# Optimization experiments

Hardware: AMD Instinct MI355X
Metric: run time of the kernel (lower is better)

The kernel has to match this reference:

```python
import jax, jax.numpy as jnp
import numpy as np

H = 8        # attention heads
EPS = 1e-5   # LayerNorm eps (torch default)


def _ln(x, g, b):
    m = x.mean(-1, keepdims=True)
    v = ((x - m) ** 2).mean(-1, keepdims=True)
    return (x - m) / jnp.sqrt(v + EPS) * g + b


def _mha(q, k, v):
    # q,k,v: [B, A, S, D] -> attend over S within each (B, A); D = H * dh
    Bq, A, S, Dm = q.shape
    dh = Dm // H
    q = q.reshape(Bq, A, S, H, dh)
    k = k.reshape(Bq, A, S, H, dh)
    v = v.reshape(Bq, A, S, H, dh)
    sc = jnp.einsum('bashe,bathe->bahst', q, k) / jnp.sqrt(jnp.asarray(dh, q.dtype))
    a = jax.nn.softmax(sc, axis=-1)
    o = jnp.einsum('bahst,bathe->bashe', a, v)
    return o.reshape(Bq, A, S, Dm)


def setup_inputs() -> dict:
    Ps, B, C, L, D, DF, PRED = 6, 16, 8, 64, 512, 2048, 96
    key = jax.random.key(0)
    ks = jax.random.split(key, 16)
    g = lambda k, s: jax.random.normal(k, s, jnp.float32) * 0.02
    D2 = (D, D)
    return dict(
        expert_x=jax.random.normal(ks[0], (Ps, B, C, L, D), jnp.float32),
        gates=jax.random.uniform(ks[1], (B, Ps), dtype=jnp.float32),
        cWq=g(ks[2], D2), cbq=jnp.zeros(D), cWk=g(ks[3], D2), cbk=jnp.zeros(D),
        cWv=g(ks[4], D2), cbv=jnp.zeros(D), cWo=g(ks[5], D2), cbo=jnp.zeros(D),
        iWq=g(ks[6], D2), ibq=jnp.zeros(D), iWk=g(ks[7], D2), ibk=jnp.zeros(D),
        iWv=g(ks[8], D2), ibv=jnp.zeros(D), iWo=g(ks[9], D2), ibo=jnp.zeros(D),
        mW1=g(ks[10], (D, DF)), mb1=jnp.zeros(DF),
        mW2=g(ks[11], (DF, D)), mb2=jnp.zeros(D),
        g1=jnp.ones(D), b1=jnp.zeros(D),
        g3=jnp.ones(D), b3=jnp.zeros(D),
        g4=jnp.ones(D), b4=jnp.zeros(D),
        hW=g(ks[12], (D, PRED)), hb=jnp.zeros(PRED),
    )


def reference(expert_x, gates,
              cWq, cbq, cWk, cbk, cWv, cbv, cWo, cbo,
              iWq, ibq, iWk, ibk, iWv, ibv, iWo, ibo,
              mW1, mb1, mW2, mb2,
              g1, b1, g3, b3, g4, b4,
              hW, hb):
    def layer(x):  # x: [B, C, L, D]
        # cross-dimension attention block (attend along L per channel)
        q = x @ cWq + cbq
        k = x @ cWk + cbk
        v = x @ cWv + cbv
        o = _mha(q, k, v) @ cWo + cbo
        x = _ln(x + o, g1, b1)
        # inter-periodicity attention block (rearrange B C L D -> B L C D, attend along C)
        q = (x @ iWq + ibq).swapaxes(1, 2)
        k = (x @ iWk + ibk).swapaxes(1, 2)
        v = (x @ iWv + ibv).swapaxes(1, 2)
        o = _mha(q, k, v).swapaxes(1, 2) @ iWo + ibo
        x = _ln(x + o, g3, b3)
        # inter-periodicity MLP (relu) + residual + norm4
        h = jnp.maximum(x @ mW1 + mb1, 0.0) @ mW2 + mb2
        return _ln(x + h, g4, b4)

    enc = jax.vmap(layer)(expert_x)                      # [Ps, B, C, L, D]
    last = enc[:, :, :, -1, :]                           # [Ps, B, C, D]: xs[i][:, :, -1:, :]
    combined = jnp.einsum('pbcd,bp->bcd', last, gates)   # gated combine over experts
    out = combined @ hW + hb                             # [B, C, pred_len]
    return out.transpose(0, 2, 1)                        # [B, pred_len, C]
```

## Files before the change

### kernel.cpp

```cpp
#include <hip/hip_runtime.h>
#include <hip/hip_bf16.h>

#define NT   49152
#define D_   512
#define DF_  2048
#define PS   6
#define BB   16
#define CC   8
#define LL   64
#define PREDN 96
#define NG   768

typedef unsigned short ushort_t;
using bf16x8 = __attribute__((ext_vector_type(8))) short;
using f32x4  = __attribute__((ext_vector_type(4))) float;

__device__ __forceinline__ float bf2f(unsigned short u) {
  return __uint_as_float((unsigned)u << 16);
}
__device__ __forceinline__ unsigned short f2bf(float f) {
  unsigned u = __float_as_uint(f);
  return (unsigned short)((u + 0x7fffu + ((u >> 16) & 1u)) >> 16);
}
__device__ __forceinline__ void unp2(int x, float& a, float& b) {
  a = __uint_as_float((unsigned)x << 16);
  b = __uint_as_float((unsigned)x & 0xffff0000u);
}
__device__ __forceinline__ void gload16(const void* g, void* l) {
  __builtin_amdgcn_global_load_lds(
      (const __attribute__((address_space(1))) unsigned*)g,
      (__attribute__((address_space(3))) unsigned*)l, 16, 0, 0);
}

template <bool RELU, bool DIAGA>
__global__ __launch_bounds__(512, 2) void gemm_mfma(
    const ushort_t* __restrict__ A,
    const ushort_t* __restrict__ Bt,
    const float* __restrict__ bias,
    ushort_t* __restrict__ C,
    int M, int N, int K) {
  __shared__ __align__(16) char smem[73728];
  short* lds = (short*)smem;
  const int tid = threadIdx.x;
  const int lane = tid & 63;
  const int w = tid >> 6;
  const int wm = w >> 1;
  const int wn = w & 1;
  const int l15 = lane & 15, l4 = lane >> 4;

  const int nbn = N >> 7;
  const int nwg = gridDim.x;
  const int qq = nwg >> 3, rr = nwg & 7;
  const int xcd = blockIdx.x & 7, within = blockIdx.x >> 3;
  const int wg = (xcd < rr ? xcd * (qq + 1) : rr * (qq + 1) + (xcd - rr) * qq) + within;
  const int bn = (wg % nbn) << 7;
  const int bm = (wg / nbn) << 8;

  const int NKT = K >> 5;

  const int ciA0 = w * 64 + lane;
  const int ciA1 = 512 + w * 64 + lane;
  const int ciB  = w * 64 + lane;
  const int rA0 = ciA0 >> 2, rA1 = ciA1 >> 2, rB = ciB >> 2;
  const int jA0 = (ciA0 & 3) ^ ((rA0 >> 1) & 3);
  const int jA1 = (ciA1 & 3) ^ ((rA1 >> 1) & 3);
  const int jB  = (ciB  & 3) ^ ((rB  >> 1) & 3);
  const ushort_t* gA0 = A + (size_t)(bm + rA0) * K + (jA0 << 3);
  const ushort_t* gA1 = A + (size_t)(bm + rA1) * K + (jA1 << 3);
  const ushort_t* gB  = Bt + (size_t)(bn + rB) * K + (jB << 3);

  auto stage = [&](int st, int sb) {
    const int k0 = st << 5;
    if (DIAGA) {
      const int kk0 = k0 + (jA0 << 3);
      const int kk1 = k0 + (jA1 << 3);
      gload16(A + ((size_t)(bm + rA0) * 8 + (kk0 >> 6)) * 512 + kk0,
              smem + sb * 24576 + w * 1024);
      gload16(A + ((size_t)(bm + rA1) * 8 + (kk1 >> 6)) * 512 + kk1,
              smem + sb * 24576 + 8192 + w * 1024);
    } else {
      gload16(gA0 + k0, smem + sb * 24576 + w * 1024);
      gload16(gA1 + k0, smem + sb * 24576 + 8192 + w * 1024);
    }
    gload16(gB + k0, smem + sb * 24576 + 16384 + w * 1024);
  };

  int aconst[4], bconst[4];
#pragma unroll
  for (int m = 0; m < 4; ++m) {
    int row = wm * 64 + m * 16 + l15;
    aconst[m] = row * 32 + ((l4 ^ ((row >> 1) & 3)) << 3);
  }
#pragma unroll
  for (int n = 0; n < 4; ++n) {
    int row = wn * 64 + n * 16 + l15;
    bconst[n] = 8192 + row * 32 + ((l4 ^ ((row >> 1) & 3)) << 3);
  }

  f32x4 acc[4][4] = {};

  stage(0, 0);
  stage(1, 1);

  int rb = 0, sb = 2;
  for (int kt = 0; kt < NKT; ++kt) {
    asm volatile("s_waitcnt vmcnt(3)" ::: "memory");
    __builtin_amdgcn_s_barrier();
    const short* buf = lds + rb * 12288;
    bf16x8 av[4], bv[4];
#pragma unroll
    for (int m = 0; m < 4; ++m) av[m] = *(const bf16x8*)(buf + aconst[m]);
#pragma unroll
    for (int n = 0; n < 4; ++n) bv[n] = *(const bf16x8*)(buf + bconst[n]);
    const int st = (kt + 2 < NKT) ? kt + 2 : NKT - 1;
    stage(st, sb);
    __builtin_amdgcn_s_barrier();
    __builtin_amdgcn_s_setprio(1);
#pragma unroll
    for (int m = 0; m < 4; ++m)
#pragma unroll
      for (int n = 0; n < 4; ++n)
        acc[m][n] = __builtin_amdgcn_mfma_f32_16x16x32_bf16(av[m], bv[n], acc[m][n], 0, 0, 0);
    __builtin_amdgcn_s_setprio(0);
    rb = (rb == 2) ? 0 : rb + 1;
    sb = (sb == 2) ? 0 : sb + 1;
  }

  asm volatile("s_waitcnt vmcnt(0)" ::: "memory");
  __syncthreads();

  float bc[4];
#pragma unroll
  for (int n = 0; n < 4; ++n) bc[n] = bias[bn + wn * 64 + n * 16 + l15];
  short* Cs = lds;
#pragma unroll
  for (int m = 0; m < 4; ++m)
#pragma unroll
    for (int n = 0; n < 4; ++n)
#pragma unroll
      for (int r2 = 0; r2 < 4; ++r2) {
        float v = acc[m][n][r2] + bc[n];
        if (RELU) v = fmaxf(v, 0.f);
        Cs[(wm * 64 + m * 16 + l4 * 4 + r2) * 136 + wn * 64 + n * 16 + l15] =
            (short)f2bf(v);
      }
  __syncthreads();
#pragma unroll
  for (int it = 0; it < 8; ++it) {
    int chunk = it * 512 + tid;
    int r = chunk >> 4;
    int c = (chunk & 15) << 3;
    int4 v = *(const int4*)(Cs + r * 136 + c);
    *(int4*)(C + (size_t)(bm + r) * N + bn + c) = v;
  }
}

__global__ __launch_bounds__(256) void prep_all(
    const float* __restrict__ ex,
    const float* __restrict__ cWq, const float* __restrict__ cWk,
    const float* __restrict__ cWv, const float* __restrict__ cWo,
    const float* __restrict__ iWq, const float* __restrict__ iWk,
    const float* __restrict__ iWv, const float* __restrict__ iWo,
    const float* __restrict__ mW1, const float* __restrict__ mW2,
    const float* __restrict__ ibq, const float* __restrict__ ibk,
    const float* __restrict__ ibv,
    ushort_t* wq, ushort_t* wv, ushort_t* wo, ushort_t* wiqkv, ushort_t* wio,
    ushort_t* w1, ushort_t* w2, ushort_t* Wqk,
    float* biqkv, float* qz, ushort_t* G768) {
  __shared__ float tile[32][33];
  const int bid = blockIdx.x;
  const int tid = threadIdx.x;

  auto do_transpose = [&](const float* W, ushort_t* Wt, int k0, int n0,
                          int Nsrc, int Kdst) {
    const int tx = tid & 31, ty = tid >> 5;
#pragma unroll
    for (int i = 0; i < 4; ++i)
      tile[ty + i * 8][tx] = W[(size_t)(k0 + ty + i * 8) * Nsrc + n0 + tx];
    __syncthreads();
#pragma unroll
    for (int i = 0; i < 4; ++i)
      Wt[(size_t)(n0 + ty + i * 8) * Kdst + k0 + tx] = f2bf(tile[tx][ty + i * 8]);
  };

  if (bid < 1792) {
    const float* srcs[7] = {cWq, cWv, cWo, iWq, iWk, iWv, iWo};
    ushort_t* dsts[7] = {wq, wv, wo, wiqkv, wiqkv + 262144, wiqkv + 524288, wio};
    const int z = bid >> 8, within = bid & 255;
    do_transpose(srcs[z], dsts[z], (within & 15) * 32, (within >> 4) * 32, 512, 512);
  } else if (bid < 2816) {
    int idx = (bid - 1792) * 256 + tid;
    int n = idx >> 6;
    int c = (idx & 63) * 8;
    int h = n >> 9, k = n & 511;
    union { unsigned short u[8]; int4 v; } pk;
    if ((c >> 6) == h) {
      float4 a = *(const float4*)(cWk + (size_t)k * 512 + c);
      float4 b = *(const float4*)(cWk + (size_t)k * 512 + c + 4);
      pk.u[0] = f2bf(a.x); pk.u[1] = f2bf(a.y); pk.u[2] = f2bf(a.z); pk.u[3] = f2bf(a.w);
      pk.u[4] = f2bf(b.x); pk.u[5] = f2bf(b.y); pk.u[6] = f2bf(b.z); pk.u[7] = f2bf(b.w);
    } else {
      pk.v = make_int4(0, 0, 0, 0);
    }
    *(int4*)(Wqk + (size_t)n * 512 + c) = pk.v;
  } else if (bid < 3840) {
    int b = bid - 2816;
    do_transpose(mW1, w1, (b & 15) * 32, (b >> 4) * 32, 2048, 512);
  } else if (bid < 4864) {
    int b = bid - 3840;
    do_transpose(mW2, w2, (b & 63) * 32, (b >> 6) * 32, 512, 2048);
  } else if (bid < 4886) {
    int i = (bid - 4864) * 256 + tid;
    if (i < 512) biqkv[i] = ibq[i];
    else if (i < 1024) biqkv[i] = ibk[i - 512];
    else if (i < 1536) biqkv[i] = ibv[i - 1024];
    else if (i < 5632) qz[i - 1536] = 0.f;
  } else {
    int g = (bid - 4886) * 4 + (tid >> 6);
    int lane = tid & 63;
    const float* src = ex + ((size_t)g * 64 + 63) * 512 + lane * 8;
    float4 a = *(const float4*)src, b = *(const float4*)(src + 4);
    union { unsigned short u[8]; int4 v; } pk;
    pk.u[0] = f2bf(a.x); pk.u[1] = f2bf(a.y); pk.u[2] = f2bf(a.z); pk.u[3] = f2bf(a.w);
    pk.u[4] = f2bf(b.x); pk.u[5] = f2bf(b.y); pk.u[6] = f2bf(b.z); pk.u[7] = f2bf(b.w);
    *(int4*)(G768 + (size_t)g * 512 + lane * 8) = pk.v;
  }
}

__global__ __launch_bounds__(512, 4) void attn_fused(
    const float* __restrict__ ex, const ushort_t* __restrict__ QW,
    ushort_t* __restrict__ Y) {
  __shared__ short xs[64][520];
  __shared__ short qws[8][520];
  __shared__ float ss[8][72];
  __shared__ float ps[8][72];
  const int g = blockIdx.x;
  const int tid = threadIdx.x;
  const int lane = tid & 63;
  const int w = tid >> 6;

  {
    const float* src = ex + (size_t)g * 64 * 512;
#pragma unroll
    for (int it = 0; it < 8; ++it) {
      int i = it * 512 + tid;
      int r = i >> 6, c = (i & 63) * 8;
      float4 a = *(const float4*)(src + r * 512 + c);
      float4 b = *(const float4*)(src + r * 512 + c + 4);
      union { unsigned short u[8]; int4 v; } pk;
      pk.u[0] = f2bf(a.x); pk.u[1] = f2bf(a.y); pk.u[2] = f2bf(a.z); pk.u[3] = f2bf(a.w);
      pk.u[4] = f2bf(b.x); pk.u[5] = f2bf(b.y); pk.u[6] = f2bf(b.z); pk.u[7] = f2bf(b.w);
      *(int4*)(&xs[r][c]) = pk.v;
    }
    int h = tid >> 6, k0 = (tid & 63) * 8;
    *(int4*)(&qws[h][k0]) = *(const int4*)(QW + (size_t)g * 4096 + tid * 8);
  }
  __syncthreads();

  if (w < 4) {
    f32x4 acc = {0.f, 0.f, 0.f, 0.f};
    const int arow = lane & 7;
    const int koff = (lane >> 4) * 8;
    const short* xrow = &xs[16 * w + (lane & 15)][0];
#pragma unroll
    for (int ks = 0; ks < 16; ++ks) {
      bf16x8 av = *(const bf16x8*)(&qws[arow][ks * 32 + koff]);
      bf16x8 bv = *(const bf16x8*)(xrow + ks * 32 + koff);
      acc = __builtin_amdgcn_mfma_f32_16x16x32_bf16(av, bv, acc, 0, 0, 0);
    }
    int t = 16 * w + (lane & 15);
    int hbase = (lane >> 4) * 4;
#pragma unroll
    for (int r = 0; r < 4; ++r) {
      int h = hbase + r;
      if (h < 8) ss[h][t] = acc[r] * 0.125f;
    }
  }
  __syncthreads();

  if (tid < 256) {
    int h = tid >> 5, t0 = tid & 31;
    float v0 = ss[h][t0], v1 = ss[h][t0 + 32];
    float mx = fmaxf(v0, v1);
#pragma unroll
    for (int o = 16; o > 0; o >>= 1) mx = fmaxf(mx, __shfl_xor(mx, o));
    float e0 = __expf(v0 - mx), e1 = __expf(v1 - mx);
    float sum = e0 + e1;
#pragma unroll
    for (int o = 16; o > 0; o >>= 1) sum += __shfl_xor(sum, o);
    float inv = 1.f / sum;
    ps[h][t0] = e0 * inv;
    ps[h][t0 + 32] = e1 * inv;
  }
  __syncthreads();

  {
    const int k0 = lane * 8;
    float acc[8] = {};
#pragma unroll
    for (int t = 0; t < 64; ++t) {
      float p = ps[w][t];
      bf16x8 xv = *(const bf16x8*)(&xs[t][k0]);
#pragma unroll
      for (int j = 0; j < 8; ++j) acc[j] += p * bf2f((unsigned short)xv[j]);
    }
    union { unsigned short u[8]; int4 v; } pk;
#pragma unroll
    for (int j = 0; j < 8; ++j) pk.u[j] = f2bf(acc[j]);
    *(int4*)(Y + ((size_t)g * 8 + w) * 512 + k0) = pk.v;
  }
}

__global__ __launch_bounds__(64) void attn_ctx(
    const ushort_t* __restrict__ QKV, ushort_t* __restrict__ O) {
  __shared__ float qs[8][72], ks[8][72], vsm[8][72], ps2[8][9];
  const int h = blockIdx.x & 7;
  const int pb = blockIdx.x >> 3;
  const int row0 = pb * 8;
  const int tid = threadIdx.x;
  {
    int c = tid >> 3, dc = (tid & 7) * 8;
    size_t r = (size_t)(row0 + c) * 1536 + h * 64 + dc;
    int4 qv = *(const int4*)(QKV + r);
    int4 kv = *(const int4*)(QKV + r + 512);
    int4 vv = *(const int4*)(QKV + r + 1024);
    unp2(qv.x, qs[c][dc + 0], qs[c][dc + 1]); unp2(qv.y, qs[c][dc + 2], qs[c][dc + 3]);
    unp2(qv.z, qs[c][dc + 4], qs[c][dc + 5]); unp2(qv.w, qs[c][dc + 6], qs[c][dc + 7]);
    unp2(kv.x, ks[c][dc + 0], ks[c][dc + 1]); unp2(kv.y, ks[c][dc + 2], ks[c][dc + 3]);
    unp2(kv.z, ks[c][dc + 4], ks[c][dc + 5]); unp2(kv.w, ks[c][dc + 6], ks[c][dc + 7]);
    unp2(vv.x, vsm[c][dc + 0], vsm[c][dc + 1]); unp2(vv.y, vsm[c][dc + 2], vsm[c][dc + 3]);
    unp2(vv.z, vsm[c][dc + 4], vsm[c][dc + 5]); unp2(vv.w, vsm[c][dc + 6], vsm[c][dc + 7]);
  }
  __syncthreads();
  {
    int i = tid >> 3, t = tid & 7;
    float s = 0.f;
#pragma unroll
    for (int d = 0; d < 64; ++d) s += qs[i][d] * ks[t][d];
    ps2[i][t] = s * 0.125f;
  }
  __syncthreads();
  if (tid < 8) {
    float mx = -1e30f;
#pragma unroll
    for (int t = 0; t < 8; ++t) mx = fmaxf(mx, ps2[tid][t]);
    float sum = 0.f;
#pragma unroll
    for (int t = 0; t < 8; ++t) { float e = __expf(ps2[tid][t] - mx); ps2[tid][t] = e; sum += e; }
    float inv = 1.f / sum;
#pragma unroll
    for (int t = 0; t < 8; ++t) ps2[tid][t] *= inv;
  }
  __syncthreads();
#pragma unroll
  for (int c = 0; c < 8; ++c) {
    float s = 0.f;
#pragma unroll
    for (int t = 0; t < 8; ++t) s += ps2[c][t] * vsm[t][tid];
    O[(size_t)(row0 + c) * 512 + h * 64 + tid] = f2bf(s);
  }
}

template <bool INF32>
__global__ __launch_bounds__(256) void add_ln(
    const void* Xin, size_t in_stride, size_t in_base,
    const ushort_t* T, ushort_t* Xout,
    const float* __restrict__ g, const float* __restrict__ b) {
  const size_t off = (size_t)blockIdx.x * D_;
  const size_t ioff = (size_t)blockIdx.x * in_stride + in_base;
  const int tid = threadIdx.x;
  float x0, x1;
  if (INF32) {
    float2 xv = ((const float2*)((const float*)Xin + ioff))[tid];
    x0 = xv.x; x1 = xv.y;
  } else {
    ushort2 xv = ((const ushort2*)((const ushort_t*)Xin + ioff))[tid];
    x0 = bf2f(xv.x); x1 = bf2f(xv.y);
  }
  ushort2 tv = ((const ushort2*)(T + off))[tid];
  x0 += bf2f(tv.x);
  x1 += bf2f(tv.y);
  float s = x0 + x1, q = x0 * x0 + x1 * x1;
#pragma unroll
  for (int o = 32; o > 0; o >>= 1) { s += __shfl_down(s, o); q += __shfl_down(q, o); }
  __shared__ float ssum[4], sqsum[4];
  if ((tid & 63) == 0) { ssum[tid >> 6] = s; sqsum[tid >> 6] = q; }
  __syncthreads();
  float S = ssum[0] + ssum[1] + ssum[2] + ssum[3];
  float Qs = sqsum[0] + sqsum[1] + sqsum[2] + sqsum[3];
  float m = S * (1.f / D_);
  float var = Qs * (1.f / D_) - m * m;
  float inv = rsqrtf(var + 1e-5f);
  float y0 = (x0 - m) * inv * g[tid * 2] + b[tid * 2];
  float y1 = (x1 - m) * inv * g[tid * 2 + 1] + b[tid * 2 + 1];
  ushort2 ov; ov.x = f2bf(y0); ov.y = f2bf(y1);
  ((ushort2*)(Xout + off))[tid] = ov;
}

__global__ __launch_bounds__(256) void final_fuse(
    const ushort_t* __restrict__ X, const ushort_t* __restrict__ P,
    const float* __restrict__ gates,
    const float* __restrict__ g4, const float* __restrict__ b4,
    const float* __restrict__ hW, const float* __restrict__ hb,
    float* __restrict__ out) {
  __shared__ float xr[D_];
  __shared__ float ssum[4], sqsum[4];
  const int bb = blockIdx.x >> 3, cc = blockIdx.x & 7;
  const int tid = threadIdx.x;
  const float gw0 = g4[tid * 2], gw1 = g4[tid * 2 + 1];
  const float bw0 = b4[tid * 2], bw1 = b4[tid * 2 + 1];
  float a0 = 0.f, a1 = 0.f;
#pragma unroll
  for (int p = 0; p < PS; ++p) {
    const size_t row = ((size_t)(p * BB + bb) * CC + cc) * D_;
    ushort2 xv = ((const ushort2*)(X + row))[tid];
    ushort2 tv = ((const ushort2*)(P + row))[tid];
    float x0 = bf2f(xv.x) + bf2f(tv.x);
    float x1 = bf2f(xv.y) + bf2f(tv.y);
    float s = x0 + x1, q = x0 * x0 + x1 * x1;
#pragma unroll
    for (int o = 32; o > 0; o >>= 1) { s += __shfl_down(s, o); q += __shfl_down(q, o); }
    if ((tid & 63) == 0) { ssum[tid >> 6] = s; sqsum[tid >> 6] = q; }
    __syncthreads();
    float S = ssum[0] + ssum[1] + ssum[2] + ssum[3];
    float Qs = sqsum[0] + sqsum[1] + sqsum[2] + sqsum[3];
    float m = S * (1.f / D_);
    float var = Qs * (1.f / D_) - m * m;
    float inv = rsqrtf(var + 1e-5f);
    float gate = gates[bb * PS + p];
    a0 += gate * ((x0 - m) * inv * gw0 + bw0);
    a1 += gate * ((x1 - m) * inv * gw1 + bw1);
    __syncthreads();
  }
  xr[tid * 2] = a0;
  xr[tid * 2 + 1] = a1;
  __syncthreads();
  if (tid < PREDN) {
    float s = hb[tid];
    for (int d = 0; d < D_; ++d) s += xr[d] * hW[d * PREDN + tid];
    out[((size_t)bb * PREDN + tid) * CC + cc] = s;
  }
}

extern "C" void kernel_launch(void* const* d_in, const int* in_sizes, int n_in,
                              void* d_out, int out_size, void* d_ws, size_t ws_size,
                              hipStream_t stream) {
  const float* ex    = (const float*)d_in[0];
  const float* gates = (const float*)d_in[1];
  const float* cWq = (const float*)d_in[2];  const float* cbq = (const float*)d_in[3];
  const float* cWk = (const float*)d_in[4];  const float* cbk = (const float*)d_in[5];
  const float* cWv = (const float*)d_in[6];  const float* cbv = (const float*)d_in[7];
  const float* cWo = (const float*)d_in[8];  const float* cbo = (const float*)d_in[9];
  const float* iWq = (const float*)d_in[10]; const float* ibq = (const float*)d_in[11];
  const float* iWk = (const float*)d_in[12]; const float* ibk = (const float*)d_in[13];
  const float* iWv = (const float*)d_in[14]; const float* ibv = (const float*)d_in[15];
  const float* iWo = (const float*)d_in[16]; const float* ibo = (const float*)d_in[17];
  const float* mW1 = (const float*)d_in[18]; const float* mb1 = (const float*)d_in[19];
  const float* mW2 = (const float*)d_in[20]; const float* mb2 = (const float*)d_in[21];
  const float* g1  = (const float*)d_in[22]; const float* b1  = (const float*)d_in[23];
  const float* g3  = (const float*)d_in[24]; const float* b3  = (const float*)d_in[25];
  const float* g4  = (const float*)d_in[26]; const float* b4  = (const float*)d_in[27];
  const float* hW  = (const float*)d_in[28]; const float* hb  = (const float*)d_in[29];
  float* out = (float*)d_out;

  ushort_t* wq    = (ushort_t*)d_ws;
  ushort_t* wv    = wq + 262144;
  ushort_t* wo    = wv + 262144;
  ushort_t* wiqkv = wo + 262144;
  ushort_t* wio   = wiqkv + 786432;
  ushort_t* w1    = wio + 262144;
  ushort_t* w2    = w1 + 1048576;
  ushort_t* Wqk   = w2 + 1048576;
  float* biqkv = (float*)(Wqk + 2097152);
  float* qz    = biqkv + 1536;
  ushort_t* G768   = (ushort_t*)(qz + 4096);
  ushort_t* Q768   = G768 + (size_t)NG * 512;
  ushort_t* QW     = Q768 + (size_t)NG * 512;
  ushort_t* Yb     = QW + (size_t)NG * 4096;
  ushort_t* Tbuf   = Yb + (size_t)NG * 4096;
  ushort_t* O768   = Tbuf + (size_t)NG * 4096;
  ushort_t* P768   = O768 + (size_t)NG * 512;
  ushort_t* X768   = P768 + (size_t)NG * 512;
  ushort_t* QKV768 = X768 + (size_t)NG * 512;
  ushort_t* H768   = QKV768 + (size_t)NG * 1536;

  prep_all<<<dim3(5078), dim3(256), 0, stream>>>(
      ex, cWq, cWk, cWv, cWo, iWq, iWk, iWv, iWo, mW1, mW2,
      ibq, ibk, ibv,
      wq, wv, wo, wiqkv, wio, w1, w2, Wqk, biqkv, qz, G768);

  gemm_mfma<false, false><<<dim3(3 * 4), dim3(512), 0, stream>>>(G768, wq, cbq, Q768, NG, 512, 512);
  gemm_mfma<false, false><<<dim3(3 * 32), dim3(512), 0, stream>>>(Q768, Wqk, qz, QW, NG, 4096, 512);
  attn_fused<<<dim3(NG), dim3(512), 0, stream>>>(ex, QW, Yb);
  gemm_mfma<false, false><<<dim3(24 * 4), dim3(512), 0, stream>>>(Yb, wv, cbv, Tbuf, NG * 8, 512, 512);
  gemm_mfma<false, true><<<dim3(3 * 4), dim3(512), 0, stream>>>(Tbuf, wo, cbo, P768, NG, 512, 512);
  add_ln<true><<<dim3(NG), dim3(256), 0, stream>>>(
      ex, (size_t)(LL * D_), (size_t)((LL - 1) * D_), P768, X768, g1, b1);

  gemm_mfma<false, false><<<dim3(3 * 12), dim3(512), 0, stream>>>(X768, wiqkv, biqkv, QKV768, NG, 1536, 512);
  attn_ctx<<<dim3(96 * 8), dim3(64), 0, stream>>>(QKV768, O768);
  gemm_mfma<false, false><<<dim3(3 * 4), dim3(512), 0, stream>>>(O768, wio, ibo, P768, NG, 512, 512);
  add_ln<false><<<dim3(NG), dim3(256), 0, stream>>>(
      X768, (size_t)D_, (size_t)0, P768, X768, g3, b3);

  gemm_mfma<true,  false><<<dim3(3 * 16), dim3(512), 0, stream>>>(X768, w1, mb1, H768, NG, 2048, 512);
  gemm_mfma<false, false><<<dim3(3 * 4), dim3(512), 0, stream>>>(H768, w2, mb2, P768, NG, 512, 2048);

  final_fuse<<<dim3(BB * CC), dim3(256), 0, stream>>>(
      X768, P768, gates, g4, b4, hW, hb, out);
}
```

Measured before the change: 181.9 us.

## Tile attn_fused over sequence with online softmax to cut LDS footprint

Restructures the fused attention kernel to process the 64-row sequence in four 16-row tiles using an online (flash-style) softmax with running max and sum per head. This shrinks the shared-memory tile from 64 rows to 16, allowing launch bounds of 8 blocks per CU instead of 4 for higher occupancy. In exchange it adds more barriers per block, leaves only one wave doing the MFMA score computation per tile, and adds rescaling work.

Result: slower. 191.0 us (+5.0%).

```diff
diff --git a/kernel.cpp b/kernel.cpp
--- a/kernel.cpp
+++ b/kernel.cpp
@@ -227,22 +227,32 @@
   }
 }
 
-__global__ __launch_bounds__(512, 4) void attn_fused(
+__global__ __launch_bounds__(512, 8) void attn_fused(
     const float* __restrict__ ex, const ushort_t* __restrict__ QW,
     ushort_t* __restrict__ Y) {
-  __shared__ short xs[64][520];
+  __shared__ short xs[16][520];
   __shared__ short qws[8][520];
-  __shared__ float ss[8][72];
-  __shared__ float ps[8][72];
+  __shared__ float ss[8][20];
+  __shared__ float ps[8][20];
+  __shared__ float scf[8], mh[8], lh[8];
   const int g = blockIdx.x;
   const int tid = threadIdx.x;
   const int lane = tid & 63;
   const int w = tid >> 6;
-
+  const int k0y = lane * 8;
+
+  if (tid < 8) { mh[tid] = -1e30f; lh[tid] = 0.f; }
   {
-    const float* src = ex + (size_t)g * 64 * 512;
-#pragma unroll
-    for (int it = 0; it < 8; ++it) {
+    int h = tid >> 6, k0 = (tid & 63) * 8;
+    *(int4*)(&qws[h][k0]) = *(const int4*)(QW + (size_t)g * 4096 + (size_t)tid * 8);
+  }
+  float acc[8] = {};
+
+  for (int T = 0; T < 4; ++T) {
+    __syncthreads();
+    const float* src = ex + ((size_t)g * 64 + T * 16) * 512;
+#pragma unroll
+    for (int it = 0; it < 2; ++it) {
       int i = it * 512 + tid;
       int r = i >> 6, c = (i & 63) * 8;
       float4 a = *(const float4*)(src + r * 512 + c);
@@ -252,62 +262,67 @@
       pk.u[4] = f2bf(b.x); pk.u[5] = f2bf(b.y); pk.u[6] = f2bf(b.z); pk.u[7] = f2bf(b.w);
       *(int4*)(&xs[r][c]) = pk.v;
     }
-    int h = tid >> 6, k0 = (tid & 63) * 8;
-    *(int4*)(&qws[h][k0]) = *(const int4*)(QW + (size_t)g * 4096 + tid * 8);
-  }
-  __syncthreads();
-
-  if (w < 4) {
-    f32x4 acc = {0.f, 0.f, 0.f, 0.f};
-    const int arow = lane & 7;
-    const int koff = (lane >> 4) * 8;
-    const short* xrow = &xs[16 * w + (lane & 15)][0];
-#pragma unroll
-    for (int ks = 0; ks < 16; ++ks) {
-      bf16x8 av = *(const bf16x8*)(&qws[arow][ks * 32 + koff]);
-      bf16x8 bv = *(const bf16x8*)(xrow + ks * 32 + koff);
-      acc = __builtin_amdgcn_mfma_f32_16x16x32_bf16(av, bv, acc, 0, 0, 0);
+    __syncthreads();
+    if (w == 0) {
+      f32x4 sacc = {0.f, 0.f, 0.f, 0.f};
+      const int arow = lane & 7;
+      const int koff = (lane >> 4) * 8;
+      const short* xrow = &xs[lane & 15][0];
+#pragma unroll
+      for (int ks = 0; ks < 16; ++ks) {
+        bf16x8 av = *(const bf16x8*)(&qws[arow][ks * 32 + koff]);
+        bf16x8 bv = *(const bf16x8*)(xrow + ks * 32 + koff);
+        sacc = __builtin_amdgcn_mfma_f32_16x16x32_bf16(av, bv, sacc, 0, 0, 0);
+      }
+      int t = lane & 15;
+      int hbase = (lane >> 4) * 4;
+#pragma unroll
+      for (int r = 0; r < 4; ++r) {
+        int h = hbase + r;
+        if (h < 8) ss[h][t] = sacc[r] * 0.125f;
+      }
     }
-    int t = 16 * w + (lane & 15);
-    int hbase = (lane >> 4) * 4;
-#pragma unroll
-    for (int r = 0; r < 4; ++r) {
-      int h = hbase + r;
-      if (h < 8) ss[h][t] = acc[r] * 0.125f;
+    __syncthreads();
+    if (tid < 128) {
+      int h = tid >> 4, t = tid & 15;
+      float v = ss[h][t];
+      float mx = v;
+#pragma unroll
+      for (int o = 8; o > 0; o >>= 1) mx = fmaxf(mx, __shfl_xor(mx, o));
+      float mold = mh[h];
+      float mnew = fmaxf(mold, mx);
+      float p = __expf(v - mnew);
+      float sum = p;
+#pragma unroll
+      for (int o = 8; o > 0; o >>= 1) sum += __shfl_xor(sum, o);
+      ps[h][t] = p;
+      if (t == 0) {
+        float sc = __expf(mold - mnew);
+        scf[h] = sc;
+        lh[h] = lh[h] * sc + sum;
+        mh[h] = mnew;
+      }
     }
-  }
-  __syncthreads();
-
-  if (tid < 256) {
-    int h = tid >> 5, t0 = tid & 31;
-    float v0 = ss[h][t0], v1 = ss[h][t0 + 32];
-    float mx = fmaxf(v0, v1);
-#pragma unroll
-    for (int o = 16; o > 0; o >>= 1) mx = fmaxf(mx, __shfl_xor(mx, o));
-    float e0 = __expf(v0 - mx), e1 = __expf(v1 - mx);
-    float sum = e0 + e1;
-#pragma unroll
-    for (int o = 16; o > 0; o >>= 1) sum += __shfl_xor(sum, o);
-    float inv = 1.f / sum;
-    ps[h][t0] = e0 * inv;
-    ps[h][t0 + 32] = e1 * inv;
-  }
-  __syncthreads();
-
+    __syncthreads();
+    {
+      float sc = scf[w];
+#pragma unroll
+      for (int j = 0; j < 8; ++j) acc[j] *= sc;
+#pragma unroll
+      for (int t = 0; t < 16; ++t) {
+        float p = ps[w][t];
+        bf16x8 xv = *(const bf16x8*)(&xs[t][k0y]);
+#pragma unroll
+        for (int j = 0; j < 8; ++j) acc[j] += p * bf2f((unsigned short)xv[j]);
+      }
+    }
+  }
   {
-    const int k0 = lane * 8;
-    float acc[8] = {};
-#pragma unroll
-    for (int t = 0; t < 64; ++t) {
-      float p = ps[w][t];
-      bf16x8 xv = *(const bf16x8*)(&xs[t][k0]);
-#pragma unroll
-      for (int j = 0; j < 8; ++j) acc[j] += p * bf2f((unsigned short)xv[j]);
-    }
+    float inv = 1.f / lh[w];
     union { unsigned short u[8]; int4 v; } pk;
 #pragma unroll
-    for (int j = 0; j < 8; ++j) pk.u[j] = f2bf(acc[j]);
-    *(int4*)(Y + ((size_t)g * 8 + w) * 512 + k0) = pk.v;
+    for (int j = 0; j < 8; ++j) pk.u[j] = f2bf(acc[j] * inv);
+    *(int4*)(Y + ((size_t)g * 8 + w) * 512 + k0y) = pk.v;
   }
 }
 
```

## Fold query projection into per-head key weights, removing one GEMM launch

Applied to the files above, without the earlier changes.

Precomputes the product of the query weight slice with each head's key weight slice (and the matching bias term) inside the prep kernel. The last-row queries then map straight to per-head key-space vectors through one GEMM instead of two. This drops a GEMM launch and an intermediate Q buffer round trip. In exchange the prep kernel does a scalar FP32 512x64x4096 weight product per call, and rounding the folded matrix to bf16 slightly changes numerics.

After: 182.6 us. No clear change (+0.4%).

```diff
diff --git a/kernel.cpp b/kernel.cpp
--- a/kernel.cpp
+++ b/kernel.cpp
@@ -162,12 +162,13 @@
     const float* __restrict__ iWq, const float* __restrict__ iWk,
     const float* __restrict__ iWv, const float* __restrict__ iWo,
     const float* __restrict__ mW1, const float* __restrict__ mW2,
-    const float* __restrict__ ibq, const float* __restrict__ ibk,
-    const float* __restrict__ ibv,
-    ushort_t* wq, ushort_t* wv, ushort_t* wo, ushort_t* wiqkv, ushort_t* wio,
-    ushort_t* w1, ushort_t* w2, ushort_t* Wqk,
-    float* biqkv, float* qz, ushort_t* G768) {
+    const float* __restrict__ cbq, const float* __restrict__ ibq,
+    const float* __restrict__ ibk, const float* __restrict__ ibv,
+    ushort_t* wv, ushort_t* wo, ushort_t* wiqkv, ushort_t* wio,
+    ushort_t* w1, ushort_t* w2, ushort_t* Mt,
+    float* biqkv, float* bias_qw, ushort_t* G768) {
   __shared__ float tile[32][33];
+  __shared__ float wk[8][64];
   const int bid = blockIdx.x;
   const int tid = threadIdx.x;
 
@@ -183,40 +184,55 @@
       Wt[(size_t)(n0 + ty + i * 8) * Kdst + k0 + tx] = f2bf(tile[tx][ty + i * 8]);
   };
 
-  if (bid < 1792) {
-    const float* srcs[7] = {cWq, cWv, cWo, iWq, iWk, iWv, iWo};
-    ushort_t* dsts[7] = {wq, wv, wo, wiqkv, wiqkv + 262144, wiqkv + 524288, wio};
+  if (bid < 1536) {
+    const float* srcs[6] = {cWv, cWo, iWq, iWk, iWv, iWo};
+    ushort_t* dsts[6] = {wv, wo, wiqkv, wiqkv + 262144, wiqkv + 524288, wio};
     const int z = bid >> 8, within = bid & 255;
     do_transpose(srcs[z], dsts[z], (within & 15) * 32, (within >> 4) * 32, 512, 512);
-  } else if (bid < 2816) {
-    int idx = (bid - 1792) * 256 + tid;
-    int n = idx >> 6;
-    int c = (idx & 63) * 8;
+  } else if (bid < 2048) {
+    const int n0 = (bid - 1536) * 8;
+    const int h = n0 >> 9;
+    const int k0 = n0 & 511;
+#pragma unroll
+    for (int e = tid; e < 512; e += 256)
+      wk[e >> 6][e & 63] = cWk[(size_t)(k0 + (e >> 6)) * 512 + h * 64 + (e & 63)];
+    __syncthreads();
+#pragma unroll
+    for (int jj = 0; jj < 2; ++jj) {
+      int j = tid + jj * 256;
+      float acc[8] = {};
+      const float* qrow = cWq + (size_t)j * 512 + h * 64;
+#pragma unroll
+      for (int d = 0; d < 64; ++d) {
+        float xq = qrow[d];
+#pragma unroll
+        for (int nn = 0; nn < 8; ++nn) acc[nn] += xq * wk[nn][d];
+      }
+#pragma unroll
+      for (int nn = 0; nn < 8; ++nn)
+        Mt[(size_t)(n0 + nn) * 512 + j] = f2bf(acc[nn]);
+    }
+  } else if (bid < 3072) {
+    int b = bid - 2048;
+    do_transpose(mW1, w1, (b & 15) * 32, (b >> 4) * 32, 2048, 512);
+  } else if (bid < 4096) {
+    int b = bid - 3072;
+    do_transpose(mW2, w2, (b & 63) * 32, (b >> 6) * 32, 512, 2048);
+  } else if (bid < 4112) {
+    int n = (bid - 4096) * 256 + tid;
     int h = n >> 9, k = n & 511;
-    union { unsigned short u[8]; int4 v; } pk;
-    if ((c >> 6) == h) {
-      float4 a = *(const float4*)(cWk + (size_t)k * 512 + c);
-      float4 b = *(const float4*)(cWk + (size_t)k * 512 + c + 4);
-      pk.u[0] = f2bf(a.x); pk.u[1] = f2bf(a.y); pk.u[2] = f2bf(a.z); pk.u[3] = f2bf(a.w);
-      pk.u[4] = f2bf(b.x); pk.u[5] = f2bf(b.y); pk.u[6] = f2bf(b.z); pk.u[7] = f2bf(b.w);
-    } else {
-      pk.v = make_int4(0, 0, 0, 0);
-    }
-    *(int4*)(Wqk + (size_t)n * 512 + c) = pk.v;
-  } else if (bid < 3840) {
-    int b = bid - 2816;
-    do_transpose(mW1, w1, (b & 15) * 32, (b >> 4) * 32, 2048, 512);
-  } else if (bid < 4864) {
-    int b = bid - 3840;
-    do_transpose(mW2, w2, (b & 63) * 32, (b >> 6) * 32, 512, 2048);
-  } else if (bid < 4886) {
-    int i = (bid - 4864) * 256 + tid;
+    float s = 0.f;
+#pragma unroll
+    for (int d = 0; d < 64; ++d)
+      s += cbq[h * 64 + d] * cWk[(size_t)k * 512 + h * 64 + d];
+    bias_qw[n] = s;
+  } else if (bid < 4118) {
+    int i = (bid - 4112) * 256 + tid;
     if (i < 512) biqkv[i] = ibq[i];
     else if (i < 1024) biqkv[i] = ibk[i - 512];
     else if (i < 1536) biqkv[i] = ibv[i - 1024];
-    else if (i < 5632) qz[i - 1536] = 0.f;
   } else {
-    int g = (bid - 4886) * 4 + (tid >> 6);
+    int g = (bid - 4118) * 4 + (tid >> 6);
     int lane = tid & 63;
     const float* src = ex + ((size_t)g * 64 + 63) * 512 + lane * 8;
     float4 a = *(const float4*)src, b = *(const float4*)(src + 4);
@@ -253,7 +269,7 @@
       *(int4*)(&xs[r][c]) = pk.v;
     }
     int h = tid >> 6, k0 = (tid & 63) * 8;
-    *(int4*)(&qws[h][k0]) = *(const int4*)(QW + (size_t)g * 4096 + tid * 8);
+    *(int4*)(&qws[h][k0]) = *(const int4*)(QW + (size_t)g * 4096 + (size_t)tid * 8);
   }
   __syncthreads();
 
@@ -463,19 +479,17 @@
   const float* hW  = (const float*)d_in[28]; const float* hb  = (const float*)d_in[29];
   float* out = (float*)d_out;
 
-  ushort_t* wq    = (ushort_t*)d_ws;
-  ushort_t* wv    = wq + 262144;
+  ushort_t* wv    = (ushort_t*)d_ws;
   ushort_t* wo    = wv + 262144;
   ushort_t* wiqkv = wo + 262144;
   ushort_t* wio   = wiqkv + 786432;
   ushort_t* w1    = wio + 262144;
   ushort_t* w2    = w1 + 1048576;
-  ushort_t* Wqk   = w2 + 1048576;
-  float* biqkv = (float*)(Wqk + 2097152);
-  float* qz    = biqkv + 1536;
-  ushort_t* G768   = (ushort_t*)(qz + 4096);
-  ushort_t* Q768   = G768 + (size_t)NG * 512;
-  ushort_t* QW     = Q768 + (size_t)NG * 512;
+  ushort_t* Mt    = w2 + 1048576;
+  float* biqkv   = (float*)(Mt + 2097152);
+  float* bias_qw = biqkv + 1536;
+  ushort_t* G768   = (ushort_t*)(bias_qw + 4096);
+  ushort_t* QW     = G768 + (size_t)NG * 512;
   ushort_t* Yb     = QW + (size_t)NG * 4096;
   ushort_t* Tbuf   = Yb + (size_t)NG * 4096;
   ushort_t* O768   = Tbuf + (size_t)NG * 4096;
@@ -484,13 +498,12 @@
   ushort_t* QKV768 = X768 + (size_t)NG * 512;
   ushort_t* H768   = QKV768 + (size_t)NG * 1536;
 
-  prep_all<<<dim3(5078), dim3(256), 0, stream>>>(
+  prep_all<<<dim3(4310), dim3(256), 0, stream>>>(
       ex, cWq, cWk, cWv, cWo, iWq, iWk, iWv, iWo, mW1, mW2,
-      ibq, ibk, ibv,
-      wq, wv, wo, wiqkv, wio, w1, w2, Wqk, biqkv, qz, G768);
-
-  gemm_mfma<false, false><<<dim3(3 * 4), dim3(512), 0, stream>>>(G768, wq, cbq, Q768, NG, 512, 512);
-  gemm_mfma<false, false><<<dim3(3 * 32), dim3(512), 0, stream>>>(Q768, Wqk, qz, QW, NG, 4096, 512);
+      cbq, ibq, ibk, ibv,
+      wv, wo, wiqkv, wio, w1, w2, Mt, biqkv, bias_qw, G768);
+
+  gemm_mfma<false, false><<<dim3(3 * 32), dim3(512), 0, stream>>>(G768, Mt, bias_qw, QW, NG, 4096, 512);
   attn_fused<<<dim3(NG), dim3(512), 0, stream>>>(ex, QW, Yb);
   gemm_mfma<false, false><<<dim3(24 * 4), dim3(512), 0, stream>>>(Yb, wv, cbv, Tbuf, NG * 8, 512, 512);
   gemm_mfma<false, true><<<dim3(3 * 4), dim3(512), 0, stream>>>(Tbuf, wo, cbo, P768, NG, 512, 512);
```
